# Optimization experiments

Hardware: AMD Instinct MI355X
Metric: run time of the kernel (lower is better)

The kernel has to match this reference:

```python
import jax, jax.numpy as jnp
import numpy as np

KERNEL_MUL = 2.0
KERNEL_NUM = 5


def _cross_entropy(logits, labels):
    logp = jax.nn.log_softmax(logits, axis=-1)
    return -jnp.take_along_axis(logp, labels[:, None], axis=-1).mean()


def _distill_loss(teacher_logits, student_logits):
    t = jax.nn.softmax(teacher_logits, axis=-1)
    return jnp.sum(-t * jax.nn.log_softmax(student_logits, axis=-1), axis=-1).mean()


def _mk_mmd(source, target):
    # Multi-kernel Gaussian MMD (standard DAN-style implementation).
    ns = source.shape[0]
    total = jnp.concatenate([source, target], axis=0)  # [ns+nt, D]
    sq = jnp.sum(total * total, axis=1)
    l2 = sq[:, None] + sq[None, :] - 2.0 * (total @ total.T)  # [n, n]
    n = total.shape[0]
    bandwidth = jnp.sum(l2) / (n * n - n)
    bandwidth = bandwidth / (KERNEL_MUL ** (KERNEL_NUM // 2))
    kernels = jnp.zeros_like(l2)
    for i in range(KERNEL_NUM):
        kernels = kernels + jnp.exp(-l2 / (bandwidth * (KERNEL_MUL ** i)))
    xx = kernels[:ns, :ns]
    yy = kernels[ns:, ns:]
    xy = kernels[:ns, ns:]
    yx = kernels[ns:, :ns]
    return jnp.mean(xx + yy - xy - yx)


def setup_inputs() -> dict:
    key = jax.random.key(0)
    k1, k2, k3, k4, k5 = jax.random.split(key, 5)
    Ns, Nt, D, C = 4096, 4096, 256, 6
    return {
        "source_feature": jax.random.normal(k1, (Ns, D), dtype=jnp.float32),
        "target_feature": jax.random.normal(k2, (Nt, D), dtype=jnp.float32),
        "source_clf": jax.random.normal(k3, (Ns, C), dtype=jnp.float32),
        "target_clf": jax.random.normal(k4, (Nt, C), dtype=jnp.float32),
        "source_label": jax.random.randint(k5, (Ns,), 0, C, dtype=jnp.int64),
    }


def reference(source_feature, target_feature, source_clf, target_clf, source_label):
    clf_loss = _cross_entropy(source_clf, source_label)

    # Pairwise euclidean distance [Ns, Nt] (cdist, p=2)
    ss = jnp.sum(source_feature * source_feature, axis=1)
    tt = jnp.sum(target_feature * target_feature, axis=1)
    d2 = ss[:, None] + tt[None, :] - 2.0 * (source_feature @ target_feature.T)
    dist = jnp.sqrt(jnp.maximum(d2, 0.0))

    min_idx = jnp.argmin(dist, axis=1)    # nearest target for each source
    min_idx_t = jnp.argmin(dist, axis=0)  # nearest source for each target

    dis_loss = _distill_loss(source_clf, target_clf[min_idx, :])
    dis_loss = dis_loss + _distill_loss(source_clf[min_idx_t, :], target_clf)

    transfer_loss = _mk_mmd(source_feature, target_feature)
    return jnp.stack([clf_loss, dis_loss, transfer_loss])
```

## Files before the change

### kernel.cpp

```cpp
#include <hip/hip_runtime.h>
#include <hip/hip_bf16.h>


#define NS 4096
#define D  256
#define C  6

typedef unsigned int u32;
typedef unsigned short u16;
typedef __attribute__((ext_vector_type(8))) short short8;
typedef __attribute__((ext_vector_type(4))) unsigned short ushort4v;
typedef __attribute__((ext_vector_type(4))) float floatx4;

#define EXP2F(x) __builtin_amdgcn_exp2f(x)

#define GLD_LDS16(g, l)                                                        \
    __builtin_amdgcn_global_load_lds(                                          \
        (const __attribute__((address_space(1))) unsigned int*)(g),            \
        (__attribute__((address_space(3))) unsigned int*)(l), 16, 0, 0)

__device__ inline u16 f2bf(float f) {
    unsigned u = __float_as_uint(f);
    return (u16)((u + 0x7FFFu + ((u >> 16) & 1u)) >> 16);
}

__global__ __launch_bounds__(256) void kA(const float* __restrict__ src,
                                          const float* __restrict__ tgt,
                                          u16* __restrict__ sb, u16* __restrict__ tb,
                                          float* __restrict__ sq,
                                          u32* __restrict__ rowkey,
                                          u32* __restrict__ colkey,
                                          double* __restrict__ accD,
                                          int* __restrict__ cnts) {
    int b = blockIdx.x, t = threadIdx.x;
    int w = t >> 6, l = t & 63;
    int r = b * 4 + w;
    const float* row = (r < NS) ? src + (size_t)r * D : tgt + (size_t)(r - NS) * D;
    u16* orow        = (r < NS) ? sb + (size_t)r * D : tb + (size_t)(r - NS) * D;
    float4 v = *(const float4*)&row[l * 4];
    ushort4v o;
    o.x = f2bf(v.x); o.y = f2bf(v.y); o.z = f2bf(v.z); o.w = f2bf(v.w);
    *(ushort4v*)&orow[l * 4] = o;
    float s = v.x * v.x + v.y * v.y + v.z * v.z + v.w * v.w;
    #pragma unroll
    for (int off = 32; off; off >>= 1) s += __shfl_down(s, off, 64);
    if (l == 0) sq[r] = s;

    int gid = b * 256 + t;
    if (gid < NS) rowkey[gid] = 0xFFFFFFFFu;
    else if (gid < 2 * NS) colkey[gid - NS] = 0xFFFFFFFFu;
    if (b == 0) {
        if (t < 8) accD[t] = 0.0;
        else if (t == 8) cnts[0] = 0;
    }
}

__global__ __launch_bounds__(256, 3) void k3_mfma(const u16* __restrict__ Sb,
                                                  const u16* __restrict__ Tb,
                                                  const float* __restrict__ sq,
                                                  double* __restrict__ accD,
                                                  u32* __restrict__ rowkey,
                                                  u32* __restrict__ colkey) {
    int idx = blockIdx.x;
    int bz, ti, tj;
    if (idx < 1024) {
        bz = 0; ti = idx >> 5; tj = idx & 31;
    } else {
        int t = idx - 1024;
        bz = 1;
        if (t >= 528) { t -= 528; bz = 2; }
        int i = (int)((65.0f - sqrtf(4225.0f - 8.0f * (float)t)) * 0.5f);
        if ((i + 1) * (64 - i) / 2 <= t) i++;
        else if (i * (65 - i) / 2 > t) i--;
        ti = i;
        tj = i + (t - i * (65 - i) / 2);
    }

    const u16* Am = (bz == 2) ? Tb : Sb;
    const u16* Bm = (bz == 1) ? Sb : Tb;
    const float* sqA = (bz == 2) ? sq + NS : sq;
    const float* sqB = (bz == 1) ? sq : sq + NS;
    int zacc = (bz == 0) ? 2 : (bz - 1);

    __shared__ __align__(16) u16 Atile[128 * 64];
    __shared__ __align__(16) u16 Btile[128 * 64];
    __shared__ float sqa_s[128], sqb_s[128];
    __shared__ u32 rminL[128], cminL[128];
    __shared__ float wsum[4];
    __shared__ float wssq[4];

    int tid = threadIdx.x;
    int w = tid >> 6, ln = tid & 63;
    int wm = w >> 1, wn = w & 1;
    int quad = ln >> 4, lrow = ln & 15;
    int row0 = ti * 128, col0 = tj * 128;

    if (tid < 128) { sqa_s[tid] = sqA[row0 + tid]; rminL[tid] = 0xFFFFFFFFu; }
    else           { sqb_s[tid - 128] = sqB[col0 + tid - 128]; cminL[tid - 128] = 0xFFFFFFFFu; }

    float ssq_p = 0.f;
    #pragma unroll
    for (int q = 0; q < 8; q++) {
        float4 v = *(const float4*)&sq[q * 1024 + tid * 4];
        ssq_p += v.x + v.y + v.z + v.w;
    }
    #pragma unroll
    for (int off = 32; off; off >>= 1) ssq_p += __shfl_down(ssq_p, off, 64);
    if (ln == 0) wssq[w] = ssq_p;

    int lr8 = ln >> 3;
    int cg  = (ln & 7) ^ lr8;

    floatx4 acc[4][4] = {};

    #pragma unroll 2
    for (int kc = 0; kc < D; kc += 64) {
        #pragma unroll
        for (int i = 0; i < 4; i++) {
            int lrb = w * 32 + i * 8;
            GLD_LDS16(Am + (size_t)(row0 + lrb + lr8) * D + kc + cg * 8,
                      &Atile[lrb * 64]);
            GLD_LDS16(Bm + (size_t)(col0 + lrb + lr8) * D + kc + cg * 8,
                      &Btile[lrb * 64]);
        }
        __syncthreads();
        #pragma unroll
        for (int ks = 0; ks < 2; ks++) {
            short8 af[4], bf4[4];
            #pragma unroll
            for (int rf = 0; rf < 4; rf++) {
                int rl = wm * 64 + rf * 16 + lrow;
                int ch = (ks * 4 + quad) ^ (lrow & 7);
                af[rf] = *(const short8*)&Atile[rl * 64 + ch * 8];
            }
            #pragma unroll
            for (int cf = 0; cf < 4; cf++) {
                int rl = wn * 64 + cf * 16 + lrow;
                int ch = (ks * 4 + quad) ^ (lrow & 7);
                bf4[cf] = *(const short8*)&Btile[rl * 64 + ch * 8];
            }
            #pragma unroll
            for (int rf = 0; rf < 4; rf++)
                #pragma unroll
                for (int cf = 0; cf < 4; cf++)
                    acc[rf][cf] = __builtin_amdgcn_mfma_f32_16x16x32_bf16(
                        af[rf], bf4[cf], acc[rf][cf], 0, 0, 0);
        }
        __syncthreads();
    }

    float sb_c[4];
    #pragma unroll
    for (int cf = 0; cf < 4; cf++)
        sb_c[cf] = sqb_s[wn * 64 + cf * 16 + lrow];

    float ssq = wssq[0] + wssq[1] + wssq[2] + wssq[3];
    float bw = (float)(2.0 * 8192.0 * (double)ssq / (8192.0 * 8192.0 - 8192.0) / 4.0);
    float nlog = -1.4426950408889634f / (bw * 16.0f);

    int rbase = row0 + wm * 64, cbase = col0 + wn * 64;
    float tsum = 0.f;

    if (bz == 0) {
        u32 ck[4];
        #pragma unroll
        for (int cf = 0; cf < 4; cf++) ck[cf] = 0xFFFFFFFFu;
        #pragma unroll
        for (int rf = 0; rf < 4; rf++) {
            float sa4[4];
            #pragma unroll
            for (int reg = 0; reg < 4; reg++)
                sa4[reg] = sqa_s[wm * 64 + rf * 16 + quad * 4 + reg];
            u32 rk[4];
            #pragma unroll
            for (int reg = 0; reg < 4; reg++) rk[reg] = 0xFFFFFFFFu;
            #pragma unroll
            for (int cf = 0; cf < 4; cf++) {
                int gj = cbase + cf * 16 + lrow;
                float sbv = sb_c[cf];
                #pragma unroll
                for (int reg = 0; reg < 4; reg++) {
                    int gi = rbase + rf * 16 + quad * 4 + reg;
                    float l2 = sa4[reg] + sbv - 2.0f * acc[rf][cf][reg];
                    float t4 = EXP2F(l2 * nlog);
                    float t3 = t4 * t4, t2 = t3 * t3, t1 = t2 * t2, t0 = t1 * t1;
                    tsum += t0 + t1 + t2 + t3 + t4;
                    u32 bits = __float_as_uint(fmaxf(l2, 0.f)) & 0xFFFFF000u;
                    rk[reg] = min(rk[reg], bits | (u32)gj);
                    ck[cf]  = min(ck[cf],  bits | (u32)gi);
                }
            }
            #pragma unroll
            for (int reg = 0; reg < 4; reg++) {
                u32 v = rk[reg];
                #pragma unroll
                for (int m = 1; m <= 8; m <<= 1)
                    v = min(v, (u32)__shfl_xor((int)v, m, 64));
                if (lrow == 0)
                    atomicMin(&rminL[wm * 64 + rf * 16 + quad * 4 + reg], v);
            }
        }
        #pragma unroll
        for (int cf = 0; cf < 4; cf++) {
            u32 v = ck[cf];
            v = min(v, (u32)__shfl_xor((int)v, 16, 64));
            v = min(v, (u32)__shfl_xor((int)v, 32, 64));
            if (quad == 0)
                atomicMin(&cminL[wn * 64 + cf * 16 + lrow], v);
        }
    } else {
        #pragma unroll
        for (int rf = 0; rf < 4; rf++) {
            float sa4[4];
            #pragma unroll
            for (int reg = 0; reg < 4; reg++)
                sa4[reg] = sqa_s[wm * 64 + rf * 16 + quad * 4 + reg];
            #pragma unroll
            for (int cf = 0; cf < 4; cf++) {
                int gj = cbase + cf * 16 + lrow;
                float sbv = sb_c[cf];
                #pragma unroll
                for (int reg = 0; reg < 4; reg++) {
                    int gi = rbase + rf * 16 + quad * 4 + reg;
                    float l2 = sa4[reg] + sbv - 2.0f * acc[rf][cf][reg];
                    float t4 = EXP2F(l2 * nlog);
                    float t3 = t4 * t4, t2 = t3 * t3, t1 = t2 * t2, t0 = t1 * t1;
                    if (ti < tj || gi < gj)
                        tsum += t0 + t1 + t2 + t3 + t4;
                }
            }
        }
    }

    #pragma unroll
    for (int off = 32; off; off >>= 1) tsum += __shfl_down(tsum, off, 64);
    if (ln == 0) wsum[w] = tsum;
    __syncthreads();
    if (tid == 0)
        atomicAdd(&accD[zacc], (double)(wsum[0] + wsum[1] + wsum[2] + wsum[3]));
    if (bz == 0) {
        if (tid < 128) atomicMin(&rowkey[row0 + tid], rminL[tid]);
        else           atomicMin(&colkey[col0 + tid - 128], cminL[tid - 128]);
    }
}

__global__ __launch_bounds__(256) void k4(const float* __restrict__ sclf,
                                          const float* __restrict__ tclf,
                                          const int* __restrict__ label,
                                          const u32* __restrict__ rowkey,
                                          const u32* __restrict__ colkey,
                                          double* __restrict__ accD,
                                          int* __restrict__ cnts,
                                          float* __restrict__ out) {
    if (blockIdx.x == 16) {
        if (threadIdx.x == 0) {
            while (atomicAdd(&cnts[0], 0) < 16) __builtin_amdgcn_s_sleep(2);
            double Sxx  = atomicAdd(&accD[0], 0.0);
            double Syy  = atomicAdd(&accD[1], 0.0);
            double Sxy  = atomicAdd(&accD[2], 0.0);
            double clfS = atomicAdd(&accD[3], 0.0);
            double disS = atomicAdd(&accD[4], 0.0);
            double ns = (double)NS;
            out[0] = (float)(clfS / ns);
            out[1] = (float)(disS / ns);
            double sum_xx = 2.0 * Sxx + ns * 5.0;
            double sum_yy = 2.0 * Syy + ns * 5.0;
            out[2] = (float)((sum_xx + sum_yy - 2.0 * Sxy) / (ns * ns));
        }
        return;
    }

    int i = blockIdx.x * 256 + threadIdx.x;
    float clf, dis = 0.f;

    const float* x = sclf + (size_t)i * C;
    float mx = x[0];
    #pragma unroll
    for (int c = 1; c < C; c++) mx = fmaxf(mx, x[c]);
    float sx = 0.f;
    #pragma unroll
    for (int c = 0; c < C; c++) sx += __expf(x[c] - mx);
    clf = mx + __logf(sx) - x[label[i]];

    {
        int j = (int)(rowkey[i] & 0xFFFu);
        const float* y = tclf + (size_t)j * C;
        float my = y[0];
        #pragma unroll
        for (int c = 1; c < C; c++) my = fmaxf(my, y[c]);
        float sy = 0.f;
        #pragma unroll
        for (int c = 0; c < C; c++) sy += __expf(y[c] - my);
        float dot = 0.f;
        #pragma unroll
        for (int c = 0; c < C; c++) dot += __expf(x[c] - mx) * y[c];
        dis += my + __logf(sy) - dot / sx;
    }
    {
        int it = (int)(colkey[i] & 0xFFFu);
        const float* xt = sclf + (size_t)it * C;
        float mt = xt[0];
        #pragma unroll
        for (int c = 1; c < C; c++) mt = fmaxf(mt, xt[c]);
        float st = 0.f;
        #pragma unroll
        for (int c = 0; c < C; c++) st += __expf(xt[c] - mt);
        const float* zz = tclf + (size_t)i * C;
        float mz = zz[0];
        #pragma unroll
        for (int c = 1; c < C; c++) mz = fmaxf(mz, zz[c]);
        float sz = 0.f;
        #pragma unroll
        for (int c = 0; c < C; c++) sz += __expf(zz[c] - mz);
        float dot2 = 0.f;
        #pragma unroll
        for (int c = 0; c < C; c++) dot2 += __expf(xt[c] - mt) * zz[c];
        dis += mz + __logf(sz) - dot2 / st;
    }

    #pragma unroll
    for (int off = 32; off; off >>= 1) {
        clf += __shfl_down(clf, off, 64);
        dis += __shfl_down(dis, off, 64);
    }
    if ((threadIdx.x & 63) == 0) {
        atomicAdd(&accD[3], (double)clf);
        atomicAdd(&accD[4], (double)dis);
    }
    __syncthreads();
    if (threadIdx.x == 0) atomicAdd(&cnts[0], 1);
}

extern "C" void kernel_launch(void* const* d_in, const int* in_sizes, int n_in,
                              void* d_out, int out_size, void* d_ws, size_t ws_size,
                              hipStream_t stream) {
    const float* src  = (const float*)d_in[0];
    const float* tgt  = (const float*)d_in[1];
    const float* sclf = (const float*)d_in[2];
    const float* tclf = (const float*)d_in[3];
    const int*   lab  = (const int*)d_in[4];
    float* out = (float*)d_out;

    char* ws = (char*)d_ws;
    u16* sb     = (u16*)ws;
    u16* tb     = sb + (size_t)NS * D;
    u32* rowkey = (u32*)(ws + 2 * (size_t)NS * D * 2);
    u32* colkey = rowkey + NS;
    float* sq   = (float*)(colkey + NS);
    double* accD = (double*)((char*)sq + 2 * NS * 4 + 64);
    int* cnts    = (int*)(accD + 8);

    kA<<<2048, 256, 0, stream>>>(src, tgt, sb, tb, sq, rowkey, colkey, accD, cnts);
    k3_mfma<<<2080, 256, 0, stream>>>(sb, tb, sq, accD, rowkey, colkey);
    k4<<<17, 256, 0, stream>>>(sclf, tclf, lab, rowkey, colkey, accD, cnts, out);
}
```

Baseline: 116.7 us.

## Fold the loss epilogue kernel into the MFMA kernel via atomic tickets

Removes the separate k4 launch. The last 16 blocks to finish the source-target tile pass (chosen by an atomic ticket) wait for all 1024 such tiles, then compute the cross-entropy and distillation terms. The final block of those 16 waits until all 2080 tiles have been counted and writes the outputs. This saves one kernel launch and the tail gap between kernels. In exchange it adds spin-waits inside the big kernel, which depend on every waited-on block being resident or already finished, and this can stall the last blocks.

```diff
diff --git a/kernel.cpp b/kernel.cpp
--- a/kernel.cpp
+++ b/kernel.cpp
@@ -51,7 +51,7 @@
     else if (gid < 2 * NS) colkey[gid - NS] = 0xFFFFFFFFu;
     if (b == 0) {
         if (t < 8) accD[t] = 0.0;
-        else if (t == 8) cnts[0] = 0;
+        else if (t < 12) cnts[t - 8] = 0;
     }
 }
 
@@ -60,7 +60,12 @@
                                                   const float* __restrict__ sq,
                                                   double* __restrict__ accD,
                                                   u32* __restrict__ rowkey,
-                                                  u32* __restrict__ colkey) {
+                                                  u32* __restrict__ colkey,
+                                                  const float* __restrict__ sclf,
+                                                  const float* __restrict__ tclf,
+                                                  const int* __restrict__ label,
+                                                  int* __restrict__ cnts,
+                                                  float* __restrict__ out) {
     int idx = blockIdx.x;
     int bz, ti, tj;
     if (idx < 1024) {
@@ -88,6 +93,7 @@
     __shared__ u32 rminL[128], cminL[128];
     __shared__ float wsum[4];
     __shared__ float wssq[4];
+    __shared__ int ticket_s;
 
     int tid = threadIdx.x;
     int w = tid >> 6, ln = tid & 63;
@@ -236,25 +242,88 @@
     for (int off = 32; off; off >>= 1) tsum += __shfl_down(tsum, off, 64);
     if (ln == 0) wsum[w] = tsum;
     __syncthreads();
+    if (tid == 0) {
+        double prev = atomicAdd(&accD[zacc],
+                                (double)(wsum[0] + wsum[1] + wsum[2] + wsum[3]));
+        if (!(prev > 1.0e300)) atomicAdd(&cnts[1], 1);
+    }
+
+    if (bz != 0) return;
+
+    if (tid < 128) atomicMin(&rowkey[row0 + tid], rminL[tid]);
+    else           atomicMin(&colkey[col0 + tid - 128], cminL[tid - 128]);
+    __syncthreads();
+    if (tid == 0) ticket_s = atomicAdd(&cnts[0], 1);
+    __syncthreads();
+    int tk = ticket_s;
+    if (tk < 1024 - 16) return;
+
     if (tid == 0)
-        atomicAdd(&accD[zacc], (double)(wsum[0] + wsum[1] + wsum[2] + wsum[3]));
-    if (bz == 0) {
-        if (tid < 128) atomicMin(&rowkey[row0 + tid], rminL[tid]);
-        else           atomicMin(&colkey[col0 + tid - 128], cminL[tid - 128]);
-    }
-}
-
-__global__ __launch_bounds__(256) void k4(const float* __restrict__ sclf,
-                                          const float* __restrict__ tclf,
-                                          const int* __restrict__ label,
-                                          const u32* __restrict__ rowkey,
-                                          const u32* __restrict__ colkey,
-                                          double* __restrict__ accD,
-                                          int* __restrict__ cnts,
-                                          float* __restrict__ out) {
-    if (blockIdx.x == 16) {
-        if (threadIdx.x == 0) {
-            while (atomicAdd(&cnts[0], 0) < 16) __builtin_amdgcn_s_sleep(2);
+        while (atomicAdd(&cnts[0], 0) < 1024) __builtin_amdgcn_s_sleep(2);
+    __syncthreads();
+
+    int i = (tk - (1024 - 16)) * 256 + tid;
+    float clf, dis = 0.f;
+    {
+        const float* x = sclf + (size_t)i * C;
+        float mx = x[0];
+        #pragma unroll
+        for (int c = 1; c < C; c++) mx = fmaxf(mx, x[c]);
+        float sx = 0.f;
+        #pragma unroll
+        for (int c = 0; c < C; c++) sx += __expf(x[c] - mx);
+        clf = mx + __logf(sx) - x[label[i]];
+
+        {
+            int j = (int)(atomicOr(&rowkey[i], 0u) & 0xFFFu);
+            const float* y = tclf + (size_t)j * C;
+            float my = y[0];
+            #pragma unroll
+            for (int c = 1; c < C; c++) my = fmaxf(my, y[c]);
+            float sy = 0.f;
+            #pragma unroll
+            for (int c = 0; c < C; c++) sy += __expf(y[c] - my);
+            float dot = 0.f;
+            #pragma unroll
+            for (int c = 0; c < C; c++) dot += __expf(x[c] - mx) * y[c];
+            dis += my + __logf(sy) - dot / sx;
+        }
+        {
+            int it = (int)(atomicOr(&colkey[i], 0u) & 0xFFFu);
+            const float* xt = sclf + (size_t)it * C;
+            float mt = xt[0];
+            #pragma unroll
+            for (int c = 1; c < C; c++) mt = fmaxf(mt, xt[c]);
+            float st = 0.f;
+            #pragma unroll
+            for (int c = 0; c < C; c++) st += __expf(xt[c] - mt);
+            const float* zz = tclf + (size_t)i * C;
+            float mz = zz[0];
+            #pragma unroll
+            for (int c = 1; c < C; c++) mz = fmaxf(mz, zz[c]);
+            float sz = 0.f;
+            #pragma unroll
+            for (int c = 0; c < C; c++) sz += __expf(zz[c] - mz);
+            float dot2 = 0.f;
+            #pragma unroll
+            for (int c = 0; c < C; c++) dot2 += __expf(xt[c] - mt) * zz[c];
+            dis += mz + __logf(sz) - dot2 / st;
+        }
+    }
+    #pragma unroll
+    for (int off = 32; off; off >>= 1) {
+        clf += __shfl_down(clf, off, 64);
+        dis += __shfl_down(dis, off, 64);
+    }
+    if (ln == 0) {
+        atomicAdd(&accD[3], (double)clf);
+        atomicAdd(&accD[4], (double)dis);
+    }
+    __syncthreads();
+    if (tid == 0) {
+        int done = atomicAdd(&cnts[2], 1);
+        if (done == 15) {
+            while (atomicAdd(&cnts[1], 0) < 2080) __builtin_amdgcn_s_sleep(2);
             double Sxx  = atomicAdd(&accD[0], 0.0);
             double Syy  = atomicAdd(&accD[1], 0.0);
             double Sxy  = atomicAdd(&accD[2], 0.0);
@@ -267,68 +336,7 @@
             double sum_yy = 2.0 * Syy + ns * 5.0;
             out[2] = (float)((sum_xx + sum_yy - 2.0 * Sxy) / (ns * ns));
         }
-        return;
-    }
-
-    int i = blockIdx.x * 256 + threadIdx.x;
-    float clf, dis = 0.f;
-
-    const float* x = sclf + (size_t)i * C;
-    float mx = x[0];
-    #pragma unroll
-    for (int c = 1; c < C; c++) mx = fmaxf(mx, x[c]);
-    float sx = 0.f;
-    #pragma unroll
-    for (int c = 0; c < C; c++) sx += __expf(x[c] - mx);
-    clf = mx + __logf(sx) - x[label[i]];
-
-    {
-        int j = (int)(rowkey[i] & 0xFFFu);
-        const float* y = tclf + (size_t)j * C;
-        float my = y[0];
-        #pragma unroll
-        for (int c = 1; c < C; c++) my = fmaxf(my, y[c]);
-        float sy = 0.f;
-        #pragma unroll
-        for (int c = 0; c < C; c++) sy += __expf(y[c] - my);
-        float dot = 0.f;
-        #pragma unroll
-        for (int c = 0; c < C; c++) dot += __expf(x[c] - mx) * y[c];
-        dis += my + __logf(sy) - dot / sx;
-    }
-    {
-        int it = (int)(colkey[i] & 0xFFFu);
-        const float* xt = sclf + (size_t)it * C;
-        float mt = xt[0];
-        #pragma unroll
-        for (int c = 1; c < C; c++) mt = fmaxf(mt, xt[c]);
-        float st = 0.f;
-        #pragma unroll
-        for (int c = 0; c < C; c++) st += __expf(xt[c] - mt);
-        const float* zz = tclf + (size_t)i * C;
-        float mz = zz[0];
-        #pragma unroll
-        for (int c = 1; c < C; c++) mz = fmaxf(mz, zz[c]);
-        float sz = 0.f;
-        #pragma unroll
-        for (int c = 0; c < C; c++) sz += __expf(zz[c] - mz);
-        float dot2 = 0.f;
-        #pragma unroll
-        for (int c = 0; c < C; c++) dot2 += __expf(xt[c] - mt) * zz[c];
-        dis += mz + __logf(sz) - dot2 / st;
-    }
-
-    #pragma unroll
-    for (int off = 32; off; off >>= 1) {
-        clf += __shfl_down(clf, off, 64);
-        dis += __shfl_down(dis, off, 64);
-    }
-    if ((threadIdx.x & 63) == 0) {
-        atomicAdd(&accD[3], (double)clf);
-        atomicAdd(&accD[4], (double)dis);
-    }
-    __syncthreads();
-    if (threadIdx.x == 0) atomicAdd(&cnts[0], 1);
+    }
 }
 
 extern "C" void kernel_launch(void* const* d_in, const int* in_sizes, int n_in,
@@ -351,6 +359,6 @@
     int* cnts    = (int*)(accD + 8);
 
     kA<<<2048, 256, 0, stream>>>(src, tgt, sb, tb, sq, rowkey, colkey, accD, cnts);
-    k3_mfma<<<2080, 256, 0, stream>>>(sb, tb, sq, accD, rowkey, colkey);
-    k4<<<17, 256, 0, stream>>>(sclf, tclf, lab, rowkey, colkey, accD, cnts, out);
+    k3_mfma<<<2080, 256, 0, stream>>>(sb, tb, sq, accD, rowkey, colkey,
+                                      sclf, tclf, lab, cnts, out);
 }
```

New measurement: 128.7 us. +10.2%, slower.
